# Performance work log

Hardware: AMD Instinct MI355X
Metric: run time of the kernel (lower is better)

Reference implementation:

```python
import jax, jax.numpy as jnp
import numpy as np

NUM_GROUPS = 32
EPS = 1e-6


def group_norm(x, scale, bias):
    # x: [b, c, l]
    b, c, l = x.shape
    xg = x.reshape(b, NUM_GROUPS, (c // NUM_GROUPS) * l)
    mean = jnp.mean(xg, axis=2, keepdims=True)
    var = jnp.var(xg, axis=2, keepdims=True)
    xn = ((xg - mean) * jax.lax.rsqrt(var + EPS)).reshape(b, c, l)
    return xn * scale[None, :, None] + bias[None, :, None]


def conv1x1(x, w, b):
    # pointwise conv: w [out_c, in_c], x [b, in_c, l]
    return jnp.einsum('oc,bcl->bol', w, x) + b[None, :, None]


def setup_inputs() -> dict:
    key = jax.random.key(0)
    ks = jax.random.split(key, 11)
    b, c, l = 4, 512, 4096
    s = 1.0 / np.sqrt(c)
    return {
        'x': jax.random.normal(ks[0], (b, c, l), jnp.float32),
        'gn_scale': jnp.ones((c,), jnp.float32),
        'gn_bias': jnp.zeros((c,), jnp.float32),
        'wq': jax.random.normal(ks[1], (c, c), jnp.float32) * s,
        'bq': jnp.zeros((c,), jnp.float32),
        'wk': jax.random.normal(ks[2], (c, c), jnp.float32) * s,
        'bk': jnp.zeros((c,), jnp.float32),
        'wv': jax.random.normal(ks[3], (c, c), jnp.float32) * s,
        'bv': jnp.zeros((c,), jnp.float32),
        'wp': jax.random.normal(ks[4], (c, c), jnp.float32) * s,
        'bp': jnp.zeros((c,), jnp.float32),
    }


def reference(x, gn_scale, gn_bias, wq, bq, wk, bk, wv, bv, wp, bp):
    h_ = group_norm(x, gn_scale, gn_bias)
    q = conv1x1(h_, wq, bq)  # [b, c, l]
    k = conv1x1(h_, wk, bk)
    v = conv1x1(h_, wv, bv)
    c = q.shape[1]
    # scores w[b,i,j] = sum_c q[b,c,i] k[b,c,j] * c^-0.5, softmax over j
    w = jnp.einsum('bci,bcj->bij', q, k) * (c ** -0.5)
    w = jax.nn.softmax(w, axis=2)
    # out[b,c,i] = sum_j w[b,i,j] v[b,c,j]
    h_ = jnp.einsum('bij,bcj->bci', w, v)
    h_ = conv1x1(h_, wp, bp)
    return x + h_
```

## Files before the change

### kernel.cpp

```cpp
#include <hip/hip_runtime.h>
#include <math.h>

#define BB 4
#define CC 512
#define LL 4096
#define NG 32
#define CPG 16
#define EPSV 1e-6f

typedef short s16x8 __attribute__((ext_vector_type(8)));
typedef __bf16 bf8v __attribute__((ext_vector_type(8)));
typedef float f32x4 __attribute__((ext_vector_type(4)));
typedef unsigned short u16;
typedef unsigned char u8;

typedef const __attribute__((address_space(1))) void g1_void;
typedef __attribute__((address_space(3))) void l3_void;

#define ASM_SBAR() asm volatile("s_barrier" ::: "memory")
#define ASM_WAITV(N) asm volatile("s_waitcnt vmcnt(" #N ")" ::: "memory")

static __device__ __forceinline__ float bf2f(u16 h) {
    unsigned int u = ((unsigned int)h) << 16;
    union { unsigned int u; float f; } c; c.u = u; return c.f;
}
static __device__ __forceinline__ u16 f2bf(float f) {
    union { float f; unsigned int u; } c; c.f = f;
    unsigned int lsb = (c.u >> 16) & 1u;
    c.u += 0x7fffu + lsb;
    return (u16)(c.u >> 16);
}
static __device__ __forceinline__ u8 f2fp8(float f) {
    int v = __builtin_amdgcn_cvt_pk_fp8_f32(f, f, 0, false);
    return (u8)(v & 0xff);
}
static __device__ __forceinline__ bf8v ld_bf8(const u16* p) {
    return *reinterpret_cast<const bf8v*>(p);
}
static __device__ __forceinline__ void gload16(const u16* g, u16* l) {
    __builtin_amdgcn_global_load_lds((g1_void*)g, (l3_void*)l, 16, 0, 0);
}
static __device__ __forceinline__ void gload16b(const u8* g, u8* l) {
    __builtin_amdgcn_global_load_lds((g1_void*)g, (l3_void*)l, 16, 0, 0);
}

__global__ __launch_bounds__(256) void wconv_kernel(const float* __restrict__ w0,
                                                    const float* __restrict__ w1,
                                                    const float* __restrict__ w2,
                                                    const float* __restrict__ w3,
                                                    u16* __restrict__ wbf) {
    int i = blockIdx.x * 256 + threadIdx.x;
    int wsel = blockIdx.y;
    const float* src = (wsel == 0) ? w0 : (wsel == 1) ? w1 : (wsel == 2) ? w2 : w3;
    float4 v = reinterpret_cast<const float4*>(src)[i];
    ushort4 o;
    o.x = f2bf(v.x); o.y = f2bf(v.y); o.z = f2bf(v.z); o.w = f2bf(v.w);
    reinterpret_cast<ushort4*>(wbf + (size_t)wsel * CC * CC)[i] = o;
}

__global__ __launch_bounds__(256) void biascat_kernel(const float* __restrict__ bq,
                                                      const float* __restrict__ bk,
                                                      const float* __restrict__ bv,
                                                      float* __restrict__ bcat,
                                                      float* __restrict__ rowsum) {
    int i = blockIdx.x * 256 + threadIdx.x;
    if (i < 3 * CC) {
        float v = (i < CC) ? bq[i] : (i < 2 * CC ? bk[i - CC] : bv[i - 2 * CC]);
        bcat[i] = v;
    }
    if (i < BB * LL) rowsum[i] = 0.f;
}

__global__ __launch_bounds__(256) void gn_stats_kernel(const float* __restrict__ x,
                                                       float2* __restrict__ stats) {
    int g = blockIdx.x, b = blockIdx.y, t = threadIdx.x;
    const float4* xp = reinterpret_cast<const float4*>(x + ((size_t)b * CC + (size_t)g * CPG) * LL);
    float s = 0.f, ss = 0.f;
    for (int it = 0; it < 64; ++it) {
        float4 v = xp[it * 256 + t];
        s += v.x + v.y + v.z + v.w;
        ss += v.x * v.x + v.y * v.y + v.z * v.z + v.w * v.w;
    }
    #pragma unroll
    for (int off = 32; off; off >>= 1) { s += __shfl_xor(s, off, 64); ss += __shfl_xor(ss, off, 64); }
    __shared__ float rs[4], rss[4];
    int wave = t >> 6, lane = t & 63;
    if (lane == 0) { rs[wave] = s; rss[wave] = ss; }
    __syncthreads();
    if (t == 0) {
        float S = rs[0] + rs[1] + rs[2] + rs[3];
        float SS = rss[0] + rss[1] + rss[2] + rss[3];
        float mean = S * (1.f / 65536.f);
        float var = SS * (1.f / 65536.f) - mean * mean;
        var = fmaxf(var, 0.f);
        stats[b * NG + g] = make_float2(mean, rsqrtf(var + EPSV));
    }
}

__global__ __launch_bounds__(256) void gn_norm_t_kernel(const float* __restrict__ x,
                                                        const float2* __restrict__ stats,
                                                        const float* __restrict__ gsc,
                                                        const float* __restrict__ gbi,
                                                        u16* __restrict__ hT) {
    int lt = blockIdx.x, ct = blockIdx.y, b = blockIdx.z;
    __shared__ u16 tile[64][72];
    int t = threadIdx.x;
    int cl0 = t >> 4, c4 = (t & 15) * 4;
    #pragma unroll
    for (int p = 0; p < 4; ++p) {
        int cl = p * 16 + cl0;
        int cg = ct * 64 + cl;
        float2 st = stats[b * NG + (cg >> 4)];
        float sc = gsc[cg] * st.y;
        float bi = gbi[cg];
        float4 v = *reinterpret_cast<const float4*>(x + ((size_t)b * CC + cg) * LL + lt * 64 + c4);
        tile[cl][c4 + 0] = f2bf((v.x - st.x) * sc + bi);
        tile[cl][c4 + 1] = f2bf((v.y - st.x) * sc + bi);
        tile[cl][c4 + 2] = f2bf((v.z - st.x) * sc + bi);
        tile[cl][c4 + 3] = f2bf((v.w - st.x) * sc + bi);
    }
    __syncthreads();
    int r = t >> 3, c8 = (t & 7) * 8;
    #pragma unroll
    for (int p = 0; p < 2; ++p) {
        int ll = p * 32 + r;
        s16x8 ov;
        #pragma unroll
        for (int j = 0; j < 8; ++j) ov[j] = (short)tile[c8 + j][ll];
        u16* hp = hT + ((size_t)b * LL + lt * 64 + ll) * CC + ct * 64 + c8;
        *reinterpret_cast<s16x8*>(hp) = ov;
    }
}

template <int MODE>
__global__ __launch_bounds__(256) void gemm_kernel(const u16* __restrict__ A, size_t asb, int lda,
                                                   const u16* __restrict__ B, size_t bsb, int ldb,
                                                   const float* __restrict__ bias,
                                                   u8* __restrict__ Oq, u8* __restrict__ Ok,
                                                   u8* __restrict__ Ov, size_t osb,
                                                   const float* __restrict__ xres,
                                                   float* __restrict__ fout, int K) {
    __shared__ u16 pool[24576];
    u8* pool8 = (u8*)pool;
    int mt = blockIdx.x, nt = blockIdx.y, b = blockIdx.z;
    int t = threadIdx.x;
    int wave = t >> 6, lane = t & 63;
    int wm = (wave >> 1) * 64, wn = (wave & 1) * 64;
    int l15 = lane & 15, quad = lane >> 4;
    f32x4 acc[4][4] = {};
    const u16* Ab = A + (size_t)b * asb + (size_t)mt * 128 * lda;
    const u16* Bb = B + (size_t)b * bsb + (size_t)nt * 128 * ldb;
    int swzg = ((lane & 3) ^ ((lane >> 2) & 3) ^ ((lane >> 4) & 3)) * 8;
    int row0 = wave * 16 + (lane >> 2);
    int row1 = 64 + row0;
    const u16* Ap0 = Ab + (size_t)row0 * lda + swzg;
    const u16* Ap1 = Ab + (size_t)row1 * lda + swzg;
    const u16* Bp0 = Bb + (size_t)row0 * ldb + swzg;
    const u16* Bp1 = Bb + (size_t)row1 * ldb + swzg;
    int wo = wave * 512;
    int swzf = (l15 & 3) ^ (l15 >> 2);
    int aoff = (wm + l15) * 32 + ((quad ^ swzf) * 8);
    int boff = (wn + l15) * 32 + ((quad ^ swzf) * 8);
    const int iters = K >> 5;
    gload16(Ap0, pool + wo);                gload16(Ap1, pool + 2048 + wo);
    gload16(Bp0, pool + 12288 + wo);        gload16(Bp1, pool + 12288 + 2048 + wo);
    gload16(Ap0 + 32, pool + 4096 + wo);    gload16(Ap1 + 32, pool + 4096 + 2048 + wo);
    gload16(Bp0 + 32, pool + 16384 + wo);   gload16(Bp1 + 32, pool + 16384 + 2048 + wo);
    int bs = 0;
    for (int i = 0; i < iters; ++i) {
        if (i + 1 < iters) { ASM_WAITV(4); } else { ASM_WAITV(0); }
        ASM_SBAR();
        const u16* As = pool + bs;
        const u16* Bs = pool + 12288 + bs;
        bf8v af[4], bfr[4];
        #pragma unroll
        for (int ii = 0; ii < 4; ++ii)
            af[ii] = ld_bf8(&As[aoff + ii * 512]);
        #pragma unroll
        for (int j = 0; j < 4; ++j)
            bfr[j] = ld_bf8(&Bs[boff + j * 512]);
        if (i + 2 < iters) {
            int kk = (i + 2) * 32;
            int nb = bs + 8192; if (nb >= 12288) nb -= 12288;
            u16* as = pool + nb; u16* bsp = pool + 12288 + nb;
            gload16(Ap0 + kk, as + wo);        gload16(Ap1 + kk, as + 2048 + wo);
            gload16(Bp0 + kk, bsp + wo);       gload16(Bp1 + kk, bsp + 2048 + wo);
        }
        __builtin_amdgcn_s_setprio(1);
        #pragma unroll
        for (int ii = 0; ii < 4; ++ii)
            #pragma unroll
            for (int j = 0; j < 4; ++j)
                acc[ii][j] = __builtin_amdgcn_mfma_f32_16x16x32_bf16(af[ii], bfr[j], acc[ii][j], 0, 0, 0);
        __builtin_amdgcn_s_setprio(0);
        bs += 4096; if (bs >= 12288) bs -= 12288;
    }
    if (MODE == 0) {
        int nt_sel = nt >> 2, ntl = nt & 3;
        if (nt_sel == 2) {
            __syncthreads();
            #pragma unroll
            for (int j = 0; j < 4; ++j) {
                float bv = bias[nt * 128 + wn + j * 16 + l15];
                #pragma unroll
                for (int i = 0; i < 4; ++i) {
                    int col = wn + j * 16 + l15;
                    int row = wm + i * 16 + quad * 4;
                    unsigned int w = __builtin_amdgcn_cvt_pk_fp8_f32(acc[i][j][0] + bv, acc[i][j][1] + bv, 0, false);
                    w = __builtin_amdgcn_cvt_pk_fp8_f32(acc[i][j][2] + bv, acc[i][j][3] + bv, w, true);
                    *reinterpret_cast<unsigned int*>(&pool8[col * 144 + row]) = w;
                }
            }
            __syncthreads();
            u8* Ob = Ov + (size_t)b * osb + (size_t)(ntl * 128) * LL + mt * 128;
            #pragma unroll
            for (int it = 0; it < 4; ++it) {
                int idx = it * 256 + t;
                int row = idx >> 3, ch = (idx & 7) * 16;
                *reinterpret_cast<float4*>(Ob + (size_t)row * LL + ch) =
                    *reinterpret_cast<const float4*>(&pool8[row * 144 + ch]);
            }
        } else {
            u8* Oc = (nt_sel == 0 ? Oq : Ok) + (size_t)b * osb
                     + (size_t)(mt * 128) * CC + ntl * 128 + wn + l15;
            #pragma unroll
            for (int j = 0; j < 4; ++j) {
                float bv = bias[nt * 128 + wn + j * 16 + l15];
                #pragma unroll
                for (int i = 0; i < 4; ++i)
                    #pragma unroll
                    for (int r = 0; r < 4; ++r) {
                        int row = wm + i * 16 + quad * 4 + r;
                        Oc[(size_t)row * CC + j * 16] = f2fp8(acc[i][j][r] + bv);
                    }
            }
        }
    } else {
        __syncthreads();
        #pragma unroll
        for (int j = 0; j < 4; ++j) {
            float bv = bias[nt * 128 + wn + j * 16 + l15];
            #pragma unroll
            for (int i = 0; i < 4; ++i)
                #pragma unroll
                for (int r = 0; r < 4; ++r) {
                    int row = wm + i * 16 + quad * 4 + r;
                    int col = wn + j * 16 + l15;
                    pool[col * 136 + row] = f2bf(acc[i][j][r] + bv);
                }
        }
        __syncthreads();
        const float* xb = xres + ((size_t)b * CC + nt * 128) * LL + mt * 128;
        float* ob = fout + ((size_t)b * CC + nt * 128) * LL + mt * 128;
        #pragma unroll
        for (int it = 0; it < 16; ++it) {
            int idx = it * 256 + t;
            int cl = idx >> 5, ch = (idx & 31) * 4;
            short4 pv = *reinterpret_cast<const short4*>(&pool[cl * 136 + ch]);
            float4 xv = *reinterpret_cast<const float4*>(xb + (size_t)cl * LL + ch);
            float4 ov;
            ov.x = xv.x + bf2f((u16)pv.x);
            ov.y = xv.y + bf2f((u16)pv.y);
            ov.z = xv.z + bf2f((u16)pv.z);
            ov.w = xv.w + bf2f((u16)pv.w);
            *reinterpret_cast<float4*>(ob + (size_t)cl * LL + ch) = ov;
        }
    }
}

template <int MODE>
__global__ __launch_bounds__(256) void gemm8_kernel(const u8* __restrict__ A, size_t asb, int lda,
                                                    const u8* __restrict__ B, size_t bsb, int ldb,
                                                    float scale,
                                                    u8* __restrict__ Out8, u16* __restrict__ OutH,
                                                    size_t osb, int Nout, int K,
                                                    float* __restrict__ rsum) {
    __shared__ u8 pool8[49152];
    int mt = blockIdx.x, nt = blockIdx.y, b = blockIdx.z;
    int t = threadIdx.x;
    int wave = t >> 6, lane = t & 63;
    int wm = (wave >> 1) * 64, wn = (wave & 1) * 64;
    int l15 = lane & 15, quad = lane >> 4;
    f32x4 acc[4][4] = {};
    int R = wave * 32 + (lane >> 1);
    int c16 = ((lane & 1) ^ (R & 1) ^ ((R >> 2) & 1)) * 16;
    const u8* Ap = A + (size_t)b * asb + (size_t)(mt * 128 + R) * lda + c16;
    const u8* Bp = B + (size_t)b * bsb + (size_t)(nt * 128 + R) * ldb + c16;
    int wo = wave * 1024;
    int p = (l15 & 1) ^ ((l15 >> 2) & 1);
    int fo = (((quad >> 1) ^ p) * 16) + (quad & 1) * 8;
    int abase = (wm + l15) * 32 + fo;
    int bbase = (wn + l15) * 32 + fo;
    const int iters = K >> 6;
    #define STG(ii, bsv) do { int kk = (ii) * 64;                          \
        gload16b(Ap + kk,      pool8 + (bsv) + wo);                        \
        gload16b(Ap + kk + 32, pool8 + (bsv) + 4096 + wo);                 \
        gload16b(Bp + kk,      pool8 + 24576 + (bsv) + wo);                \
        gload16b(Bp + kk + 32, pool8 + 24576 + (bsv) + 4096 + wo); } while (0)
    float invl[4][4];
    if (MODE == 2) {
        #pragma unroll
        for (int i = 0; i < 4; ++i)
            #pragma unroll
            for (int r = 0; r < 4; ++r)
                invl[i][r] = 1.f / rsum[(size_t)b * LL + mt * 128 + wm + i * 16 + quad * 4 + r];
    }
    STG(0, 0);
    STG(1, 8192);
    int bs = 0;
    for (int i = 0; i < iters; ++i) {
        if (i + 1 < iters) { ASM_WAITV(4); } else { ASM_WAITV(0); }
        ASM_SBAR();
        const u8* As = pool8 + bs;
        const u8* Bs = pool8 + 24576 + bs;
        long af0[4], bf0[4], af1[4], bf1[4];
        #pragma unroll
        for (int ii = 0; ii < 4; ++ii) {
            af0[ii] = *reinterpret_cast<const long*>(As + abase + ii * 512);
            af1[ii] = *reinterpret_cast<const long*>(As + 4096 + abase + ii * 512);
        }
        #pragma unroll
        for (int j = 0; j < 4; ++j) {
            bf0[j] = *reinterpret_cast<const long*>(Bs + bbase + j * 512);
            bf1[j] = *reinterpret_cast<const long*>(Bs + 4096 + bbase + j * 512);
        }
        if (i + 2 < iters) {
            int nb = bs + 16384; if (nb >= 24576) nb -= 24576;
            STG(i + 2, nb);
        }
        __builtin_amdgcn_s_setprio(1);
        #pragma unroll
        for (int ii = 0; ii < 4; ++ii)
            #pragma unroll
            for (int j = 0; j < 4; ++j)
                acc[ii][j] = __builtin_amdgcn_mfma_f32_16x16x32_fp8_fp8(af0[ii], bf0[j], acc[ii][j], 0, 0, 0);
        #pragma unroll
        for (int ii = 0; ii < 4; ++ii)
            #pragma unroll
            for (int j = 0; j < 4; ++j)
                acc[ii][j] = __builtin_amdgcn_mfma_f32_16x16x32_fp8_fp8(af1[ii], bf1[j], acc[ii][j], 0, 0, 0);
        __builtin_amdgcn_s_setprio(0);
        bs += 8192; if (bs >= 24576) bs -= 24576;
    }
    #undef STG
    if (MODE == 1) {
        u8* Ob = Out8 + (size_t)b * osb + (size_t)(mt * 128) * Nout + nt * 128 + wn + l15;
        #pragma unroll
        for (int i = 0; i < 4; ++i) {
            #pragma unroll
            for (int r = 0; r < 4; ++r) {
                int row = wm + i * 16 + quad * 4 + r;
                u8* rp = Ob + (size_t)row * Nout;
                float part = 0.f;
                #pragma unroll
                for (int j = 0; j < 4; ++j) {
                    float v = __expf(acc[i][j][r] * scale - 3.0f);
                    part += v;
                    rp[j * 16] = f2fp8(v);
                }
                part += __shfl_xor(part, 1, 64);
                part += __shfl_xor(part, 2, 64);
                part += __shfl_xor(part, 4, 64);
                part += __shfl_xor(part, 8, 64);
                if (l15 == 0)
                    atomicAdd(rsum + (size_t)b * LL + mt * 128 + row, part);
            }
        }
    } else {
        __syncthreads();
        u16* poolh = (u16*)pool8;
        #pragma unroll
        for (int j = 0; j < 4; ++j)
            #pragma unroll
            for (int i = 0; i < 4; ++i)
                #pragma unroll
                for (int r = 0; r < 4; ++r) {
                    int row = wm + i * 16 + quad * 4 + r;
                    int col = wn + j * 16 + l15;
                    poolh[row * 136 + col] = f2bf(acc[i][j][r] * invl[i][r]);
                }
        __syncthreads();
        u16* Ob = OutH + (size_t)b * osb + (size_t)(mt * 128) * Nout + nt * 128;
        #pragma unroll
        for (int it = 0; it < 8; ++it) {
            int idx = it * 256 + t;
            int row = idx >> 4, ch = (idx & 15) * 8;
            s16x8 val = *reinterpret_cast<const s16x8*>(&poolh[row * 136 + ch]);
            *reinterpret_cast<s16x8*>(Ob + (size_t)row * Nout + ch) = val;
        }
    }
}

extern "C" void kernel_launch(void* const* d_in, const int* in_sizes, int n_in,
                              void* d_out, int out_size, void* d_ws, size_t ws_size,
                              hipStream_t stream) {
    const float* x   = (const float*)d_in[0];
    const float* gsc = (const float*)d_in[1];
    const float* gbi = (const float*)d_in[2];
    const float* wq  = (const float*)d_in[3];
    const float* bq  = (const float*)d_in[4];
    const float* wk  = (const float*)d_in[5];
    const float* bk  = (const float*)d_in[6];
    const float* wv  = (const float*)d_in[7];
    const float* bv  = (const float*)d_in[8];
    const float* wp  = (const float*)d_in[9];
    const float* bp  = (const float*)d_in[10];
    float* out = (float*)d_out;

    char* ws = (char*)d_ws;
    const size_t SZ   = (size_t)BB * LL * CC * 2;
    const size_t QSZ  = (size_t)BB * LL * CC;
    const size_t WQSZ = (size_t)4 * CC * CC * 2;
    const size_t RSZ  = (size_t)BB * LL * 4;
    u16* bufA = (u16*)(ws);
    u8*  q8   = (u8*)(ws + SZ);
    u8*  k8   = (u8*)(ws + SZ + QSZ);
    u8*  v8   = (u8*)(ws + SZ + 2 * QSZ);
    u16* wbf  = (u16*)(ws + SZ + 3 * QSZ);
    float2* stats = (float2*)(ws + SZ + 3 * QSZ + WQSZ);
    float* bcat   = (float*)(ws + SZ + 3 * QSZ + WQSZ + 4096);
    float* rowsum = (float*)(ws + SZ + 3 * QSZ + WQSZ + 4096 + 8192);
    u8* S8 = (u8*)(ws + SZ + 3 * QSZ + WQSZ + 4096 + 8192 + RSZ);
    const float scale = 0.044194173824159216f;
    const size_t BLC = (size_t)LL * CC;

    wconv_kernel<<<dim3(256, 4), 256, 0, stream>>>(wq, wk, wv, wp, wbf);
    biascat_kernel<<<dim3(64), 256, 0, stream>>>(bq, bk, bv, bcat, rowsum);
    gn_stats_kernel<<<dim3(NG, BB), 256, 0, stream>>>(x, stats);
    gn_norm_t_kernel<<<dim3(64, 8, BB), 256, 0, stream>>>(x, stats, gsc, gbi, bufA);
    gemm_kernel<0><<<dim3(32, 12, BB), 256, 0, stream>>>(bufA, BLC, CC, wbf, 0, CC, bcat,
                                                         q8, k8, v8, BLC, nullptr, nullptr, CC);
    gemm8_kernel<1><<<dim3(32, 32, BB), 256, 0, stream>>>(q8, BLC, CC, k8, BLC, CC, scale,
                                                          S8, nullptr, (size_t)LL * LL, LL, CC, rowsum);
    gemm8_kernel<2><<<dim3(32, 4, BB), 256, 0, stream>>>(S8, (size_t)LL * LL, LL, v8, BLC, LL, 1.f,
                                                         nullptr, bufA, BLC, CC, LL, rowsum);
    gemm_kernel<3><<<dim3(32, 4, BB), 256, 0, stream>>>(bufA, BLC, CC, wbf + 3 * CC * CC, 0, CC,
                                                        bp, nullptr, nullptr, nullptr, 0, x, out, CC);
}
```

Before: 305.8 us.

## Switch fp8 attention GEMM to 32x32x64 scaled MFMA with new fragment layout

Replaces the 16x16x32 fp8 MFMA inner loop (32 instructions per k-step) with four 32x32x64 f8f6f4 scaled MFMAs using unit scales, reworking LDS fragment addressing and both epilogues to the 32x32 accumulator layout. The goal is fewer MFMA issues and fewer LDS reads per k-step, which raises matrix-core throughput per instruction. Row-sum reductions now span 32 lanes, and MODE 2 loads the reciprocal normalizers in the epilogue instead of before the loop. The risk is in the swizzled LDS addressing and the output row mapping, which must exactly match the new MFMA operand and result layout.

```diff
diff --git a/kernel.cpp b/kernel.cpp
--- a/kernel.cpp
+++ b/kernel.cpp
@@ -11,6 +11,9 @@
 typedef short s16x8 __attribute__((ext_vector_type(8)));
 typedef __bf16 bf8v __attribute__((ext_vector_type(8)));
 typedef float f32x4 __attribute__((ext_vector_type(4)));
+typedef float f32x16 __attribute__((ext_vector_type(16)));
+typedef int i32x4 __attribute__((ext_vector_type(4)));
+typedef int i32x8 __attribute__((ext_vector_type(8)));
 typedef unsigned short u16;
 typedef unsigned char u8;
 
@@ -37,6 +40,14 @@
 static __device__ __forceinline__ bf8v ld_bf8(const u16* p) {
     return *reinterpret_cast<const bf8v*>(p);
 }
+static __device__ __forceinline__ i32x8 ld32(const u8* plo, const u8* phi) {
+    i32x4 lo = *reinterpret_cast<const i32x4*>(plo);
+    i32x4 hi = *reinterpret_cast<const i32x4*>(phi);
+    return __builtin_shufflevector(lo, hi, 0, 1, 2, 3, 4, 5, 6, 7);
+}
+#define MFMA_SC(a, b, c) \
+    __builtin_amdgcn_mfma_scale_f32_32x32x64_f8f6f4(a, b, c, 0, 0, 0, 0x7f, 0, 0x7f)
+
 static __device__ __forceinline__ void gload16(const u16* g, u16* l) {
     __builtin_amdgcn_global_load_lds((g1_void*)g, (l3_void*)l, 16, 0, 0);
 }
@@ -280,31 +291,27 @@
     int t = threadIdx.x;
     int wave = t >> 6, lane = t & 63;
     int wm = (wave >> 1) * 64, wn = (wave & 1) * 64;
-    int l15 = lane & 15, quad = lane >> 4;
-    f32x4 acc[4][4] = {};
+    int l31 = lane & 31, hsel = lane >> 5;
+    f32x16 acc[2][2] = {};
     int R = wave * 32 + (lane >> 1);
     int c16 = ((lane & 1) ^ (R & 1) ^ ((R >> 2) & 1)) * 16;
     const u8* Ap = A + (size_t)b * asb + (size_t)(mt * 128 + R) * lda + c16;
     const u8* Bp = B + (size_t)b * bsb + (size_t)(nt * 128 + R) * ldb + c16;
     int wo = wave * 1024;
-    int p = (l15 & 1) ^ ((l15 >> 2) & 1);
-    int fo = (((quad >> 1) ^ p) * 16) + (quad & 1) * 8;
-    int abase = (wm + l15) * 32 + fo;
-    int bbase = (wn + l15) * 32 + fo;
+    int ra = wm + l31;
+    int rb = wn + l31;
+    int sa = (ra & 1) ^ ((ra >> 2) & 1);
+    int sb = (rb & 1) ^ ((rb >> 2) & 1);
+    int a_lo = hsel * 4096 + ra * 32 + sa * 16;
+    int a_hi = hsel * 4096 + ra * 32 + 16 - sa * 16;
+    int b_lo = hsel * 4096 + rb * 32 + sb * 16;
+    int b_hi = hsel * 4096 + rb * 32 + 16 - sb * 16;
     const int iters = K >> 6;
     #define STG(ii, bsv) do { int kk = (ii) * 64;                          \
         gload16b(Ap + kk,      pool8 + (bsv) + wo);                        \
         gload16b(Ap + kk + 32, pool8 + (bsv) + 4096 + wo);                 \
         gload16b(Bp + kk,      pool8 + 24576 + (bsv) + wo);                \
         gload16b(Bp + kk + 32, pool8 + 24576 + (bsv) + 4096 + wo); } while (0)
-    float invl[4][4];
-    if (MODE == 2) {
-        #pragma unroll
-        for (int i = 0; i < 4; ++i)
-            #pragma unroll
-            for (int r = 0; r < 4; ++r)
-                invl[i][r] = 1.f / rsum[(size_t)b * LL + mt * 128 + wm + i * 16 + quad * 4 + r];
-    }
     STG(0, 0);
     STG(1, 8192);
     int bs = 0;
@@ -313,72 +320,69 @@
         ASM_SBAR();
         const u8* As = pool8 + bs;
         const u8* Bs = pool8 + 24576 + bs;
-        long af0[4], bf0[4], af1[4], bf1[4];
-        #pragma unroll
-        for (int ii = 0; ii < 4; ++ii) {
-            af0[ii] = *reinterpret_cast<const long*>(As + abase + ii * 512);
-            af1[ii] = *reinterpret_cast<const long*>(As + 4096 + abase + ii * 512);
-        }
-        #pragma unroll
-        for (int j = 0; j < 4; ++j) {
-            bf0[j] = *reinterpret_cast<const long*>(Bs + bbase + j * 512);
-            bf1[j] = *reinterpret_cast<const long*>(Bs + 4096 + bbase + j * 512);
-        }
+        i32x8 a0 = ld32(As + a_lo, As + a_hi);
+        i32x8 a1 = ld32(As + 1024 + a_lo, As + 1024 + a_hi);
+        i32x8 b0 = ld32(Bs + b_lo, Bs + b_hi);
+        i32x8 b1 = ld32(Bs + 1024 + b_lo, Bs + 1024 + b_hi);
         if (i + 2 < iters) {
             int nb = bs + 16384; if (nb >= 24576) nb -= 24576;
             STG(i + 2, nb);
         }
         __builtin_amdgcn_s_setprio(1);
-        #pragma unroll
-        for (int ii = 0; ii < 4; ++ii)
-            #pragma unroll
-            for (int j = 0; j < 4; ++j)
-                acc[ii][j] = __builtin_amdgcn_mfma_f32_16x16x32_fp8_fp8(af0[ii], bf0[j], acc[ii][j], 0, 0, 0);
-        #pragma unroll
-        for (int ii = 0; ii < 4; ++ii)
-            #pragma unroll
-            for (int j = 0; j < 4; ++j)
-                acc[ii][j] = __builtin_amdgcn_mfma_f32_16x16x32_fp8_fp8(af1[ii], bf1[j], acc[ii][j], 0, 0, 0);
+        acc[0][0] = MFMA_SC(a0, b0, acc[0][0]);
+        acc[0][1] = MFMA_SC(a0, b1, acc[0][1]);
+        acc[1][0] = MFMA_SC(a1, b0, acc[1][0]);
+        acc[1][1] = MFMA_SC(a1, b1, acc[1][1]);
         __builtin_amdgcn_s_setprio(0);
         bs += 8192; if (bs >= 24576) bs -= 24576;
     }
     #undef STG
     if (MODE == 1) {
-        u8* Ob = Out8 + (size_t)b * osb + (size_t)(mt * 128) * Nout + nt * 128 + wn + l15;
-        #pragma unroll
-        for (int i = 0; i < 4; ++i) {
-            #pragma unroll
-            for (int r = 0; r < 4; ++r) {
-                int row = wm + i * 16 + quad * 4 + r;
-                u8* rp = Ob + (size_t)row * Nout;
-                float part = 0.f;
+        u8* Ob = Out8 + (size_t)b * osb + (size_t)(mt * 128) * Nout + nt * 128 + wn + l31;
+        float* rbase = rsum + (size_t)b * LL + mt * 128;
+        #pragma unroll
+        for (int i = 0; i < 2; ++i) {
+            #pragma unroll
+            for (int rg = 0; rg < 4; ++rg) {
                 #pragma unroll
-                for (int j = 0; j < 4; ++j) {
-                    float v = __expf(acc[i][j][r] * scale - 3.0f);
-                    part += v;
-                    rp[j * 16] = f2fp8(v);
+                for (int rr = 0; rr < 4; ++rr) {
+                    int reg = rg * 4 + rr;
+                    int row = wm + i * 32 + rr + 8 * rg + 4 * hsel;
+                    float v0 = __expf(acc[i][0][reg] * scale - 3.0f);
+                    float v1 = __expf(acc[i][1][reg] * scale - 3.0f);
+                    u8* rp = Ob + (size_t)row * Nout;
+                    rp[0]  = f2fp8(v0);
+                    rp[32] = f2fp8(v1);
+                    float part = v0 + v1;
+                    part += __shfl_xor(part, 1, 64);
+                    part += __shfl_xor(part, 2, 64);
+                    part += __shfl_xor(part, 4, 64);
+                    part += __shfl_xor(part, 8, 64);
+                    part += __shfl_xor(part, 16, 64);
+                    if (l31 == 0)
+                        atomicAdd(rbase + row, part);
                 }
-                part += __shfl_xor(part, 1, 64);
-                part += __shfl_xor(part, 2, 64);
-                part += __shfl_xor(part, 4, 64);
-                part += __shfl_xor(part, 8, 64);
-                if (l15 == 0)
-                    atomicAdd(rsum + (size_t)b * LL + mt * 128 + row, part);
             }
         }
     } else {
         __syncthreads();
         u16* poolh = (u16*)pool8;
-        #pragma unroll
-        for (int j = 0; j < 4; ++j)
-            #pragma unroll
-            for (int i = 0; i < 4; ++i)
+        const float* rbase = rsum + (size_t)b * LL + mt * 128;
+        #pragma unroll
+        for (int i = 0; i < 2; ++i)
+            #pragma unroll
+            for (int rg = 0; rg < 4; ++rg) {
+                int row0 = wm + i * 32 + 8 * rg + 4 * hsel;
+                float4 rv = *reinterpret_cast<const float4*>(rbase + row0);
+                float iv[4] = {1.f / rv.x, 1.f / rv.y, 1.f / rv.z, 1.f / rv.w};
                 #pragma unroll
-                for (int r = 0; r < 4; ++r) {
-                    int row = wm + i * 16 + quad * 4 + r;
-                    int col = wn + j * 16 + l15;
-                    poolh[row * 136 + col] = f2bf(acc[i][j][r] * invl[i][r]);
+                for (int rr = 0; rr < 4; ++rr) {
+                    int reg = rg * 4 + rr;
+                    int row = row0 + rr;
+                    poolh[row * 136 + wn + l31]      = f2bf(acc[i][0][reg] * iv[rr]);
+                    poolh[row * 136 + wn + 32 + l31] = f2bf(acc[i][1][reg] * iv[rr]);
                 }
+            }
         __syncthreads();
         u16* Ob = OutH + (size_t)b * osb + (size_t)(mt * 128) * Nout + nt * 128;
         #pragma unroll
```

Result: no change. 309.7 us (+1.3%).
